# Optimization experiments

Hardware: AMD Instinct MI355X
Metric: run time of the kernel (lower is better)

Reference implementation:

```python
import jax, jax.numpy as jnp
import numpy as np

B, S, E = 2, 2048, 2048
H, D = 16, 128
I = 8192
EPS = 1e-5


def layernorm(x, w, b):
    mu = jnp.mean(x, axis=-1, keepdims=True)
    var = jnp.mean(jnp.square(x - mu), axis=-1, keepdims=True)
    return (x - mu) * jax.lax.rsqrt(var + EPS) * w + b


def setup_inputs() -> dict:
    key = jax.random.key(0)
    ks = jax.random.split(key, 6)
    s = 0.02
    return {
        "x": jax.random.normal(ks[0], (B, S, E), jnp.float32),
        "ln1_w": jnp.ones((E,), jnp.float32),
        "ln1_b": jnp.zeros((E,), jnp.float32),
        "Wqkv": jax.random.normal(ks[1], (E, 3 * E), jnp.float32) * s,
        "Wo": jax.random.normal(ks[2], (E, E), jnp.float32) * s,
        "ln2_w": jnp.ones((E,), jnp.float32),
        "ln2_b": jnp.zeros((E,), jnp.float32),
        "W1": jax.random.normal(ks[3], (E, I), jnp.float32) * s,
        "W2": jax.random.normal(ks[4], (I, E), jnp.float32) * s,
    }


def reference(x, ln1_w, ln1_b, Wqkv, Wo, ln2_w, ln2_b, W1, W2):
    scale = D ** -0.5
    # --- attention sublayer (pre-LN) ---
    h = layernorm(x, ln1_w, ln1_b)
    qkv = (h @ Wqkv).reshape(B, S, 3, H, D)
    q, k, v = [jnp.moveaxis(qkv[:, :, i], 1, 2) for i in range(3)]  # [B,H,S,D]
    scores = jnp.einsum("bhqd,bhkd->bhqk", q, k) * scale
    causal = jnp.triu(jnp.ones((S, S), bool), k=1)
    scores = jnp.where(causal, -jnp.inf, scores)
    attn = jax.nn.softmax(scores, axis=-1)
    out = jnp.einsum("bhqk,bhkd->bqhd", attn, v).reshape(B, S, E)
    x = x + out @ Wo
    # --- FFN sublayer (pre-LN) ---
    h = layernorm(x, ln2_w, ln2_b)
    x = x + jax.nn.gelu(h @ W1, approximate=True) @ W2
    return x
```

## Files before the change

### kernel.cpp

```cpp
#include <hip/hip_runtime.h>
#include <hip/hip_bf16.h>

#define B_ 2
#define S_ 2048
#define E_ 2048
#define H_ 16
#define D_ 128
#define I_ 8192
#define T_ (B_*S_)

typedef __attribute__((ext_vector_type(8))) short bf16x8;
typedef __attribute__((ext_vector_type(8))) unsigned short us8;
typedef __attribute__((ext_vector_type(4))) float f32x4;

__device__ __forceinline__ unsigned short f2bf(float f) {
  union { float f; unsigned int u; } c; c.f = f;
  unsigned int u = c.u;
  unsigned int r = (u + 0x7fffu + ((u >> 16) & 1u)) >> 16;
  return (unsigned short)r;
}

__device__ __forceinline__ void gload16(const void* g, void* l) {
  __builtin_amdgcn_global_load_lds((const __attribute__((address_space(1))) void*)g,
                                   (__attribute__((address_space(3))) void*)l, 16, 0, 0);
}

__global__ void transpose_w(const float* __restrict__ in, unsigned short* __restrict__ out,
                            int K, int N) {
  __shared__ float tile[32][33];
  const int n0 = blockIdx.x * 32, k0 = blockIdx.y * 32;
  const int tx = threadIdx.x, ty = threadIdx.y;
#pragma unroll
  for (int j = 0; j < 4; ++j) {
    int k = k0 + ty + j * 8;
    tile[ty + j * 8][tx] = in[(size_t)k * N + n0 + tx];
  }
  __syncthreads();
#pragma unroll
  for (int j = 0; j < 4; ++j) {
    int n = n0 + ty + j * 8;
    out[(size_t)n * K + k0 + tx] = f2bf(tile[tx][ty + j * 8]);
  }
}

__global__ void ln_kernel(const float* __restrict__ x, const float* __restrict__ w,
                          const float* __restrict__ b, unsigned short* __restrict__ out) {
  const int row = blockIdx.x;
  const int tid = threadIdx.x;
  const int wid = tid >> 6, lane = tid & 63;
  const float4* xr = (const float4*)(x + (size_t)row * E_);
  float4 v0 = xr[tid * 2], v1 = xr[tid * 2 + 1];
  float s  = v0.x + v0.y + v0.z + v0.w + v1.x + v1.y + v1.z + v1.w;
  float sq = v0.x*v0.x + v0.y*v0.y + v0.z*v0.z + v0.w*v0.w
           + v1.x*v1.x + v1.y*v1.y + v1.z*v1.z + v1.w*v1.w;
#pragma unroll
  for (int off = 32; off > 0; off >>= 1) {
    s  += __shfl_xor(s, off);
    sq += __shfl_xor(sq, off);
  }
  __shared__ float red[8];
  if (lane == 0) { red[wid] = s; red[wid + 4] = sq; }
  __syncthreads();
  s  = red[0] + red[1] + red[2] + red[3];
  sq = red[4] + red[5] + red[6] + red[7];
  const float mu  = s * (1.0f / E_);
  const float var = sq * (1.0f / E_) - mu * mu;
  const float rstd = rsqrtf(var + 1e-5f);
  const float4* w4 = (const float4*)w + tid * 2;
  const float4* b4 = (const float4*)b + tid * 2;
  float4 w0 = w4[0], w1 = w4[1], bb0 = b4[0], bb1 = b4[1];
  us8 o;
  o[0] = f2bf((v0.x - mu) * rstd * w0.x + bb0.x);
  o[1] = f2bf((v0.y - mu) * rstd * w0.y + bb0.y);
  o[2] = f2bf((v0.z - mu) * rstd * w0.z + bb0.z);
  o[3] = f2bf((v0.w - mu) * rstd * w0.w + bb0.w);
  o[4] = f2bf((v1.x - mu) * rstd * w1.x + bb1.x);
  o[5] = f2bf((v1.y - mu) * rstd * w1.y + bb1.y);
  o[6] = f2bf((v1.z - mu) * rstd * w1.z + bb1.z);
  o[7] = f2bf((v1.w - mu) * rstd * w1.w + bb1.w);
  *(us8*)(&out[(size_t)row * E_ + tid * 8]) = o;
}

template<int EPI>
__global__ void gemm_bt(const unsigned short* __restrict__ A,
                        const unsigned short* __restrict__ Bt,
                        void* __restrict__ Cout,
                        const float* __restrict__ resid,
                        int M, int N, int K) {
  __shared__ __align__(16) unsigned short As[128 * 32];
  __shared__ __align__(16) unsigned short Bs[128 * 32];
  const int gn = N >> 7;
  const int nwg = (M >> 7) * gn;
  const int cpx = nwg >> 3;
  const int bid = blockIdx.x;
  const int swz = (bid & 7) * cpx + (bid >> 3);
  const int bm = swz / gn, bn = swz % gn;
  const int tid = threadIdx.x;
  const int wid = tid >> 6, lane = tid & 63;
  const int fr = lane & 15, kg = lane >> 4;
  const int wr = wid >> 1, wc = wid & 1;

  const int c0 = wid * 2;
  const unsigned short* gA = A  + (size_t)(bm * 128 + c0 * 16 + (lane >> 2)) * K + (lane & 3) * 8;
  const unsigned short* gB = Bt + (size_t)(bn * 128 + c0 * 16 + (lane >> 2)) * K + (lane & 3) * 8;
  unsigned short* lA = &As[c0 * 512];
  unsigned short* lB = &Bs[c0 * 512];

  const unsigned short* rA = &As[(wr * 64 + fr) * 32 + kg * 8];
  const unsigned short* rB = &Bs[(wc * 64 + fr) * 32 + kg * 8];

  f32x4 acc[4][4] = {};
  const int nk = K >> 5;
  for (int kt = 0; kt < nk; ++kt) {
    __syncthreads();
    gload16(gA,                 lA);
    gload16(gA + 16 * (size_t)K, lA + 512);
    gload16(gB,                 lB);
    gload16(gB + 16 * (size_t)K, lB + 512);
    gA += 32; gB += 32;
    __syncthreads();
    bf16x8 af[4], bfr[4];
#pragma unroll
    for (int m = 0; m < 4; ++m) af[m]  = *(const bf16x8*)(rA + m * 16 * 32);
#pragma unroll
    for (int n = 0; n < 4; ++n) bfr[n] = *(const bf16x8*)(rB + n * 16 * 32);
#pragma unroll
    for (int m = 0; m < 4; ++m)
#pragma unroll
      for (int n = 0; n < 4; ++n)
        acc[m][n] = __builtin_amdgcn_mfma_f32_16x16x32_bf16(af[m], bfr[n], acc[m][n], 0, 0, 0);
  }

  const int row0 = bm * 128 + wr * 64;
  const int col0 = bn * 128 + wc * 64;
#pragma unroll
  for (int m = 0; m < 4; ++m) {
#pragma unroll
    for (int n = 0; n < 4; ++n) {
#pragma unroll
      for (int r = 0; r < 4; ++r) {
        const int row = row0 + m * 16 + kg * 4 + r;
        const int col = col0 + n * 16 + fr;
        const size_t idx = (size_t)row * N + col;
        const float v = acc[m][n][r];
        if constexpr (EPI == 0) {
          ((unsigned short*)Cout)[idx] = f2bf(v);
        } else if constexpr (EPI == 1) {
          const float u = 0.7978845608028654f * (v + 0.044715f * v * v * v);
          const float gel = 0.5f * v * (1.0f + tanhf(u));
          ((unsigned short*)Cout)[idx] = f2bf(gel);
        } else {
          ((float*)Cout)[idx] = v + resid[idx];
        }
      }
    }
  }
}

#define DSR(dst, addr, off) \
  asm volatile("ds_read_b128 %0, %1 offset:%c2" : "=v"(dst) : "v"(addr), "i"(off))
#define LDA4_(aad, kh, mh) \
  DSR(af[0], aad, (kh)*16384 + (mh)*4096 + 0);    \
  DSR(af[1], aad, (kh)*16384 + (mh)*4096 + 1024); \
  DSR(af[2], aad, (kh)*16384 + (mh)*4096 + 2048); \
  DSR(af[3], aad, (kh)*16384 + (mh)*4096 + 3072)
#define LDB4_(bbd, kh) \
  DSR(bq[0], bbd, (kh)*16384 + 0);    \
  DSR(bq[1], bbd, (kh)*16384 + 1024); \
  DSR(bq[2], bbd, (kh)*16384 + 2048); \
  DSR(bq[3], bbd, (kh)*16384 + 3072)
#define FENCE_ do { asm volatile("s_waitcnt lgkmcnt(0)"); \
                    __builtin_amdgcn_sched_barrier(0); } while (0)
#define REG_(op, c, kh) (((((op) * 2 + (c)) * 2 + (kh))) * 8192)

template<int EPI>
__global__ __launch_bounds__(512, 2)
void gemm256(const unsigned short* __restrict__ A,
             const unsigned short* __restrict__ Bt,
             void* __restrict__ Cout,
             const float* __restrict__ resid,
             int M, int N, int K) {
  __shared__ __align__(16) unsigned short lds[65536];
  const int gn = N >> 8;
  const int nwg = (M >> 8) * gn;
  const int cpx = nwg >> 3;
  const int bid = blockIdx.x;
  const int swz = (bid & 7) * cpx + (bid >> 3);
  const int bm = swz / gn, bn = swz % gn;
  const int tid = threadIdx.x;
  const int w = tid >> 6, lane = tid & 63;
  const int fr = lane & 15, kg = lane >> 4;
  const int wr = w >> 2, wc = w & 3;

  const int cc_s = (tid & 7) ^ ((tid >> 3) & 7);
  const int row_s = 2 * (tid >> 3) + (cc_s >> 2);
  const int ks_s = (cc_s & 3) * 8;
  const unsigned short* gA = A  + (size_t)(bm * 256 + row_s) * K + ks_s;
  const unsigned short* gB = Bt + (size_t)(bn * 256 + row_s) * K + ks_s;

  const int lread = (fr >> 1) * 64 + ((((fr & 1) * 4 + kg) ^ (fr >> 1)) * 8);
  const int aA0 = wr * 8192 + lread * 2;
  const int aA1 = 32768 + wr * 8192 + lread * 2;
  const int bB0 = 65536 + wc * 4096 + lread * 2;
  const int bB1 = 65536 + 32768 + wc * 4096 + lread * 2;

  auto STG = [&](const unsigned short* g, unsigned short* l) {
    gload16(g, l);
    gload16(g + (size_t)128 * K, l + 4096);
  };

  f32x4 acc[8][4] = {};
  bf16x8 af[4], bq[4];

  auto MM16 = [&](int mh) {
    __builtin_amdgcn_s_setprio(1);
#pragma unroll
    for (int m = 0; m < 4; ++m)
#pragma unroll
      for (int n = 0; n < 4; ++n)
        acc[mh * 4 + m][n] =
            __builtin_amdgcn_mfma_f32_16x16x32_bf16(af[m], bq[n], acc[mh * 4 + m][n], 0, 0, 0);
    __builtin_amdgcn_s_setprio(0);
  };

#define KTILE(AAD, BBD, DB, kt)  {                                        \
    const bool pf = (kt) + 1 < nk;                                        \
    const unsigned short* gAn = gA + (size_t)((kt) + 1) * 64;             \
    const unsigned short* gBn = gB + (size_t)((kt) + 1) * 64;             \
    LDA4_(AAD, 0, 0); LDB4_(BBD, 0);                                      \
    if (pf) STG(gAn, &lds[REG_(0, DB, 0) + w * 512]);                     \
    __builtin_amdgcn_s_barrier(); FENCE_;                                 \
    MM16(0);                                                              \
    __builtin_amdgcn_s_barrier();                                         \
    LDA4_(AAD, 0, 1);                                                     \
    if (pf) STG(gBn, &lds[REG_(1, DB, 0) + w * 512]);                     \
    __builtin_amdgcn_s_barrier(); FENCE_;                                 \
    MM16(1);                                                              \
    if (pf) { asm volatile("s_waitcnt vmcnt(4)" ::: "memory"); }          \
    else    { asm volatile("s_waitcnt vmcnt(0)" ::: "memory"); }          \
    __builtin_amdgcn_s_barrier();                                         \
    LDA4_(AAD, 1, 0); LDB4_(BBD, 1);                                      \
    if (pf) STG(gAn + 32, &lds[REG_(0, DB, 1) + w * 512]);                \
    __builtin_amdgcn_s_barrier(); FENCE_;                                 \
    MM16(0);                                                              \
    __builtin_amdgcn_s_barrier();                                         \
    LDA4_(AAD, 1, 1);                                                     \
    if (pf) STG(gBn + 32, &lds[REG_(1, DB, 1) + w * 512]);                \
    __builtin_amdgcn_s_barrier(); FENCE_;                                 \
    MM16(1);                                                              \
    if (pf) { asm volatile("s_waitcnt vmcnt(4)" ::: "memory"); }          \
    __builtin_amdgcn_s_barrier();                                         \
  }

  const int nk = K >> 6;
  STG(gA,      &lds[REG_(0, 0, 0) + w * 512]);
  STG(gB,      &lds[REG_(1, 0, 0) + w * 512]);
  STG(gA + 32, &lds[REG_(0, 0, 1) + w * 512]);
  STG(gB + 32, &lds[REG_(1, 0, 1) + w * 512]);
  asm volatile("s_waitcnt vmcnt(4)" ::: "memory");
  __builtin_amdgcn_s_barrier();

  for (int kt2 = 0; kt2 < (nk >> 1); ++kt2) {
    KTILE(aA0, bB0, 1, 2 * kt2);
    KTILE(aA1, bB1, 0, 2 * kt2 + 1);
  }
#undef KTILE

  const int row0 = bm * 256 + wr * 128;
  const int col0 = bn * 256 + wc * 64;
#pragma unroll
  for (int m = 0; m < 8; ++m) {
#pragma unroll
    for (int n = 0; n < 4; ++n) {
#pragma unroll
      for (int r = 0; r < 4; ++r) {
        const int row = row0 + m * 16 + kg * 4 + r;
        const int col = col0 + n * 16 + fr;
        const size_t idx = (size_t)row * N + col;
        const float v = acc[m][n][r];
        if constexpr (EPI == 0) {
          ((unsigned short*)Cout)[idx] = f2bf(v);
        } else if constexpr (EPI == 1) {
          const float u = 0.7978845608028654f * (v + 0.044715f * v * v * v);
          const float gel = 0.5f * v * (1.0f + tanhf(u));
          ((unsigned short*)Cout)[idx] = f2bf(gel);
        } else {
          ((float*)Cout)[idx] = v + resid[idx];
        }
      }
    }
  }
}

__global__ void extract_vT(const unsigned short* __restrict__ qkv, unsigned short* __restrict__ vT) {
  __shared__ unsigned short tile[32][34];
  const int bh = blockIdx.z;
  const int b = bh >> 4, h = bh & 15;
  const int s0 = blockIdx.y * 32, d0 = blockIdx.x * 32;
  const int tx = threadIdx.x, ty = threadIdx.y;
#pragma unroll
  for (int j = 0; j < 4; ++j) {
    int s = s0 + ty + j * 8;
    tile[ty + j * 8][tx] = qkv[(size_t)(b * S_ + s) * 6144 + 4096 + h * 128 + d0 + tx];
  }
  __syncthreads();
#pragma unroll
  for (int j = 0; j < 4; ++j) {
    int d = d0 + ty + j * 8;
    vT[((size_t)bh * 128 + d) * 2048 + s0 + tx] = tile[tx][ty + j * 8];
  }
}

__global__ __launch_bounds__(256, 2)
void attn_kernel(const unsigned short* __restrict__ qkv,
                 const unsigned short* __restrict__ vT,
                 unsigned short* __restrict__ outp) {
  __shared__ __align__(16) unsigned short Ks[64 * 128];
  __shared__ __align__(16) unsigned short Vts[128 * 64];
  __shared__ __align__(16) unsigned short Ps[4 * 16 * 40];
  const int qt = blockIdx.x;
  const int bh = blockIdx.y;
  const int b = bh >> 4, h = bh & 15;
  const int tid = threadIdx.x, wid = tid >> 6, lane = tid & 63;
  const int fr = lane & 15, g = lane >> 4;

  const unsigned short* qptr = qkv + (size_t)(b * S_ + qt * 64 + wid * 16 + fr) * 6144 + h * 128;
  bf16x8 qf[4];
#pragma unroll
  for (int dc = 0; dc < 4; ++dc) qf[dc] = *(const bf16x8*)(qptr + dc * 32 + g * 8);

  float m0[4], l0[4];
#pragma unroll
  for (int r = 0; r < 4; ++r) { m0[r] = -1e30f; l0[r] = 0.0f; }
  f32x4 acc[8] = {};

  const unsigned short* kbase = qkv + (size_t)(b * S_) * 6144 + 2048 + h * 128;
  const unsigned short* vbase = vT + (size_t)bh * 128 * 2048;
  unsigned short* Pw = &Ps[wid * 640];
  const float scale = 0.08838834764831845f;

  us8 kreg[4], vreg[4];
#pragma unroll
  for (int j = 0; j < 4; ++j) {
    const int cc = tid + 256 * j;
    kreg[j] = *(const us8*)(kbase + (size_t)(cc >> 4) * 6144 + (cc & 15) * 8);
    vreg[j] = *(const us8*)(vbase + (size_t)(cc >> 3) * 2048 + (cc & 7) * 8);
  }

  for (int kt = 0; kt <= qt; ++kt) {
    __syncthreads();
#pragma unroll
    for (int j = 0; j < 4; ++j) {
      const int cc = tid + 256 * j;
      const int krow = cc >> 4, kcp = cc & 15;
      *(us8*)(&Ks[krow * 128 + ((kcp * 8) ^ ((krow & 7) << 3))]) = kreg[j];
      const int drow = cc >> 3, vcp = cc & 7;
      *(us8*)(&Vts[drow * 64 + ((vcp * 8) ^ ((drow & 7) << 3))]) = vreg[j];
    }
    if (kt < qt) {
#pragma unroll
      for (int j = 0; j < 4; ++j) {
        const int cc = tid + 256 * j;
        kreg[j] = *(const us8*)(kbase + (size_t)((kt + 1) * 64 + (cc >> 4)) * 6144 + (cc & 15) * 8);
        vreg[j] = *(const us8*)(vbase + (size_t)(cc >> 3) * 2048 + (kt + 1) * 64 + (cc & 7) * 8);
      }
    }
    __syncthreads();

    f32x4 sc[4] = {};
    __builtin_amdgcn_s_setprio(1);
#pragma unroll
    for (int dc = 0; dc < 4; ++dc) {
#pragma unroll
      for (int sub = 0; sub < 4; ++sub) {
        const int row = sub * 16 + fr;
        bf16x8 kf = *(const bf16x8*)(&Ks[row * 128 + ((dc * 32 + g * 8) ^ ((row & 7) << 3))]);
        sc[sub] = __builtin_amdgcn_mfma_f32_16x16x32_bf16(qf[dc], kf, sc[sub], 0, 0, 0);
      }
    }
    __builtin_amdgcn_s_setprio(0);

    float p[4][4];
    const bool diag = (kt == qt);
#pragma unroll
    for (int sub = 0; sub < 4; ++sub) {
#pragma unroll
      for (int r = 0; r < 4; ++r) {
        float v = sc[sub][r] * scale;
        if (diag && (sub * 16 + fr > wid * 16 + g * 4 + r)) v = -1e30f;
        p[sub][r] = v;
      }
    }
    float corr[4];
#pragma unroll
    for (int r = 0; r < 4; ++r) {
      float mx = fmaxf(fmaxf(p[0][r], p[1][r]), fmaxf(p[2][r], p[3][r]));
#pragma unroll
      for (int off = 1; off < 16; off <<= 1) mx = fmaxf(mx, __shfl_xor(mx, off));
      const float mn = fmaxf(m0[r], mx);
      corr[r] = __expf(m0[r] - mn);
      m0[r] = mn;
      float rs = 0.0f;
#pragma unroll
      for (int sub = 0; sub < 4; ++sub) { p[sub][r] = __expf(p[sub][r] - mn); rs += p[sub][r]; }
#pragma unroll
      for (int off = 1; off < 16; off <<= 1) rs += __shfl_xor(rs, off);
      l0[r] = l0[r] * corr[r] + rs;
    }
#pragma unroll
    for (int dt = 0; dt < 8; ++dt)
#pragma unroll
      for (int r = 0; r < 4; ++r) acc[dt][r] *= corr[r];

#pragma unroll
    for (int half = 0; half < 2; ++half) {
#pragma unroll
      for (int s2 = 0; s2 < 2; ++s2)
#pragma unroll
        for (int r = 0; r < 4; ++r)
          Pw[(g * 4 + r) * 40 + s2 * 16 + fr] = f2bf(p[half * 2 + s2][r]);
      bf16x8 pf = *(const bf16x8*)(&Pw[fr * 40 + g * 8]);
      __builtin_amdgcn_s_setprio(1);
#pragma unroll
      for (int dt = 0; dt < 8; ++dt) {
        const int row = dt * 16 + fr;
        bf16x8 vf = *(const bf16x8*)(&Vts[row * 64 + ((half * 32 + g * 8) ^ ((row & 7) << 3))]);
        acc[dt] = __builtin_amdgcn_mfma_f32_16x16x32_bf16(pf, vf, acc[dt], 0, 0, 0);
      }
      __builtin_amdgcn_s_setprio(0);
    }
  }

  float inv[4];
#pragma unroll
  for (int r = 0; r < 4; ++r) inv[r] = 1.0f / l0[r];
#pragma unroll
  for (int dt = 0; dt < 8; ++dt)
#pragma unroll
    for (int r = 0; r < 4; ++r) {
      const size_t row = (size_t)(b * S_ + qt * 64 + wid * 16 + g * 4 + r);
      outp[row * E_ + h * 128 + dt * 16 + fr] = f2bf(acc[dt][r] * inv[r]);
    }
}

extern "C" void kernel_launch(void* const* d_in, const int* in_sizes, int n_in,
                              void* d_out, int out_size, void* d_ws, size_t ws_size,
                              hipStream_t stream) {
  (void)in_sizes; (void)n_in; (void)out_size; (void)ws_size;
  const float* x    = (const float*)d_in[0];
  const float* ln1w = (const float*)d_in[1];
  const float* ln1b = (const float*)d_in[2];
  const float* Wqkv = (const float*)d_in[3];
  const float* Wo   = (const float*)d_in[4];
  const float* ln2w = (const float*)d_in[5];
  const float* ln2b = (const float*)d_in[6];
  const float* W1   = (const float*)d_in[7];
  const float* W2   = (const float*)d_in[8];
  float* out = (float*)d_out;
  char* ws = (char*)d_ws;

  unsigned short* WqkvT = (unsigned short*)(ws + 0);
  unsigned short* WoT   = (unsigned short*)(ws + 25165824);
  unsigned short* W1T   = (unsigned short*)(ws + 33554432);
  unsigned short* W2T   = (unsigned short*)(ws + 67108864);
  unsigned short* qkvb  = (unsigned short*)(ws + 100663296);
  unsigned short* vTb   = (unsigned short*)(ws + 150994944);
  unsigned short* gbuf  = (unsigned short*)(ws + 100663296);
  unsigned short* hbuf  = (unsigned short*)(ws + 167772160);
  float*          x1    = (float*)         (ws + 184549376);

  const dim3 tb(32, 8);
  hipLaunchKernelGGL(transpose_w, dim3(6144 / 32, 2048 / 32), tb, 0, stream, Wqkv, WqkvT, 2048, 6144);
  hipLaunchKernelGGL(transpose_w, dim3(2048 / 32, 2048 / 32), tb, 0, stream, Wo,   WoT,   2048, 2048);
  hipLaunchKernelGGL(transpose_w, dim3(8192 / 32, 2048 / 32), tb, 0, stream, W1,   W1T,   2048, 8192);
  hipLaunchKernelGGL(transpose_w, dim3(2048 / 32, 8192 / 32), tb, 0, stream, W2,   W2T,   8192, 2048);

  hipLaunchKernelGGL(ln_kernel, dim3(T_), dim3(256), 0, stream, x, ln1w, ln1b, hbuf);
  hipLaunchKernelGGL((gemm_bt<0>), dim3(32 * 48), dim3(256), 0, stream,
                     hbuf, WqkvT, (void*)qkvb, (const float*)nullptr, T_, 6144, 2048);
  hipLaunchKernelGGL(extract_vT, dim3(4, 64, 32), tb, 0, stream, qkvb, vTb);
  hipLaunchKernelGGL(attn_kernel, dim3(S_ / 64, B_ * H_), dim3(256), 0, stream, qkvb, vTb, hbuf);
  hipLaunchKernelGGL((gemm_bt<2>), dim3(32 * 16), dim3(256), 0, stream,
                     hbuf, WoT, (void*)x1, x, T_, 2048, 2048);
  hipLaunchKernelGGL(ln_kernel, dim3(T_), dim3(256), 0, stream, x1, ln2w, ln2b, hbuf);
  hipLaunchKernelGGL((gemm256<1>), dim3(16 * 32), dim3(512), 0, stream,
                     hbuf, W1T, (void*)gbuf, (const float*)nullptr, T_, 8192, 2048);
  hipLaunchKernelGGL((gemm_bt<2>), dim3(32 * 16), dim3(256), 0, stream,
                     gbuf, W2T, (void*)out, x1, T_, 2048, 8192);
}
```

Before: 766.3 us.

## Restructure gemm256 into 4-stage k32 ring pipeline; use it for QKV projection

The gemm256 main loop is rebuilt as a four-buffer ring of 32-wide K units with three units prefetched ahead. This removes most of the per-half-tile barriers and uses only a vmcnt wait plus one barrier per unit. The QKV projection is also switched from the 128-tile gemm_bt kernel to the 256x256 gemm256 kernel. The deeper pipeline is meant to hide global-load latency and cut synchronization overhead, but it depends on careful buffer reuse ordering, which could race when a slot is refilled.

```diff
diff --git a/kernel.cpp b/kernel.cpp
--- a/kernel.cpp
+++ b/kernel.cpp
@@ -159,19 +159,6 @@
 
 #define DSR(dst, addr, off) \
   asm volatile("ds_read_b128 %0, %1 offset:%c2" : "=v"(dst) : "v"(addr), "i"(off))
-#define LDA4_(aad, kh, mh) \
-  DSR(af[0], aad, (kh)*16384 + (mh)*4096 + 0);    \
-  DSR(af[1], aad, (kh)*16384 + (mh)*4096 + 1024); \
-  DSR(af[2], aad, (kh)*16384 + (mh)*4096 + 2048); \
-  DSR(af[3], aad, (kh)*16384 + (mh)*4096 + 3072)
-#define LDB4_(bbd, kh) \
-  DSR(bq[0], bbd, (kh)*16384 + 0);    \
-  DSR(bq[1], bbd, (kh)*16384 + 1024); \
-  DSR(bq[2], bbd, (kh)*16384 + 2048); \
-  DSR(bq[3], bbd, (kh)*16384 + 3072)
-#define FENCE_ do { asm volatile("s_waitcnt lgkmcnt(0)"); \
-                    __builtin_amdgcn_sched_barrier(0); } while (0)
-#define REG_(op, c, kh) (((((op) * 2 + (c)) * 2 + (kh))) * 8192)
 
 template<int EPI>
 __global__ __launch_bounds__(512, 2)
@@ -199,15 +186,8 @@
   const unsigned short* gB = Bt + (size_t)(bn * 256 + row_s) * K + ks_s;
 
   const int lread = (fr >> 1) * 64 + ((((fr & 1) * 4 + kg) ^ (fr >> 1)) * 8);
-  const int aA0 = wr * 8192 + lread * 2;
-  const int aA1 = 32768 + wr * 8192 + lread * 2;
-  const int bB0 = 65536 + wc * 4096 + lread * 2;
-  const int bB1 = 65536 + 32768 + wc * 4096 + lread * 2;
-
-  auto STG = [&](const unsigned short* g, unsigned short* l) {
-    gload16(g, l);
-    gload16(g + (size_t)128 * K, l + 4096);
-  };
+  const int la = wr * 8192 + lread * 2;
+  const int lb = 16384 + wc * 4096 + lread * 2;
 
   f32x4 acc[8][4] = {};
   bf16x8 af[4], bq[4];
@@ -222,49 +202,56 @@
             __builtin_amdgcn_mfma_f32_16x16x32_bf16(af[m], bq[n], acc[mh * 4 + m][n], 0, 0, 0);
     __builtin_amdgcn_s_setprio(0);
   };
-
-#define KTILE(AAD, BBD, DB, kt)  {                                        \
-    const bool pf = (kt) + 1 < nk;                                        \
-    const unsigned short* gAn = gA + (size_t)((kt) + 1) * 64;             \
-    const unsigned short* gBn = gB + (size_t)((kt) + 1) * 64;             \
-    LDA4_(AAD, 0, 0); LDB4_(BBD, 0);                                      \
-    if (pf) STG(gAn, &lds[REG_(0, DB, 0) + w * 512]);                     \
-    __builtin_amdgcn_s_barrier(); FENCE_;                                 \
+  auto STGA = [&](int u, int buf) {
+    const unsigned short* g = gA + (size_t)u * 32;
+    unsigned short* d = &lds[buf * 16384 + w * 512];
+    gload16(g, d); gload16(g + (size_t)128 * K, d + 4096);
+  };
+  auto STGB = [&](int u, int buf) {
+    const unsigned short* g = gB + (size_t)u * 32;
+    unsigned short* d = &lds[buf * 16384 + 8192 + w * 512];
+    gload16(g, d); gload16(g + (size_t)128 * K, d + 4096);
+  };
+
+#define UNIT(J, PF, GATE) {                                               \
+    const int aA = la + (J) * 32768;                                      \
+    const int aB = lb + (J) * 32768;                                      \
+    DSR(af[0], aA, 0);    DSR(af[1], aA, 1024);                           \
+    DSR(af[2], aA, 2048); DSR(af[3], aA, 3072);                           \
+    DSR(bq[0], aB, 0);    DSR(bq[1], aB, 1024);                           \
+    DSR(bq[2], aB, 2048); DSR(bq[3], aB, 3072);                           \
+    if (PF) STGA(ku + (J) + 3, ((J) + 3) & 3);                            \
+    asm volatile("s_waitcnt lgkmcnt(0)");                                 \
+    __builtin_amdgcn_sched_barrier(0);                                    \
     MM16(0);                                                              \
-    __builtin_amdgcn_s_barrier();                                         \
-    LDA4_(AAD, 0, 1);                                                     \
-    if (pf) STG(gBn, &lds[REG_(1, DB, 0) + w * 512]);                     \
-    __builtin_amdgcn_s_barrier(); FENCE_;                                 \
+    DSR(af[0], aA, 4096); DSR(af[1], aA, 5120);                           \
+    DSR(af[2], aA, 6144); DSR(af[3], aA, 7168);                           \
+    if (PF) STGB(ku + (J) + 3, ((J) + 3) & 3);                            \
+    asm volatile("s_waitcnt lgkmcnt(0)");                                 \
+    __builtin_amdgcn_sched_barrier(0);                                    \
     MM16(1);                                                              \
-    if (pf) { asm volatile("s_waitcnt vmcnt(4)" ::: "memory"); }          \
-    else    { asm volatile("s_waitcnt vmcnt(0)" ::: "memory"); }          \
-    __builtin_amdgcn_s_barrier();                                         \
-    LDA4_(AAD, 1, 0); LDB4_(BBD, 1);                                      \
-    if (pf) STG(gAn + 32, &lds[REG_(0, DB, 1) + w * 512]);                \
-    __builtin_amdgcn_s_barrier(); FENCE_;                                 \
-    MM16(0);                                                              \
-    __builtin_amdgcn_s_barrier();                                         \
-    LDA4_(AAD, 1, 1);                                                     \
-    if (pf) STG(gBn + 32, &lds[REG_(1, DB, 1) + w * 512]);                \
-    __builtin_amdgcn_s_barrier(); FENCE_;                                 \
-    MM16(1);                                                              \
-    if (pf) { asm volatile("s_waitcnt vmcnt(4)" ::: "memory"); }          \
-    __builtin_amdgcn_s_barrier();                                         \
-  }
-
-  const int nk = K >> 6;
-  STG(gA,      &lds[REG_(0, 0, 0) + w * 512]);
-  STG(gB,      &lds[REG_(1, 0, 0) + w * 512]);
-  STG(gA + 32, &lds[REG_(0, 0, 1) + w * 512]);
-  STG(gB + 32, &lds[REG_(1, 0, 1) + w * 512]);
-  asm volatile("s_waitcnt vmcnt(4)" ::: "memory");
+    if ((GATE) == 8)      asm volatile("s_waitcnt vmcnt(8)" ::: "memory");\
+    else if ((GATE) == 4) asm volatile("s_waitcnt vmcnt(4)" ::: "memory");\
+    else if ((GATE) == 0) asm volatile("s_waitcnt vmcnt(0)" ::: "memory");\
+    if ((GATE) >= 0) __builtin_amdgcn_s_barrier();                        \
+  }
+
+  const int nu = K >> 5;
+  STGA(0, 0); STGB(0, 0);
+  STGA(1, 1); STGB(1, 1);
+  STGA(2, 2); STGB(2, 2);
+  asm volatile("s_waitcnt vmcnt(8)" ::: "memory");
   __builtin_amdgcn_s_barrier();
 
-  for (int kt2 = 0; kt2 < (nk >> 1); ++kt2) {
-    KTILE(aA0, bB0, 1, 2 * kt2);
-    KTILE(aA1, bB1, 0, 2 * kt2 + 1);
-  }
-#undef KTILE
+  int ku = 0;
+  for (int it = 0; it < (nu >> 2) - 1; ++it, ku += 4) {
+    UNIT(0, true, 8); UNIT(1, true, 8); UNIT(2, true, 8); UNIT(3, true, 8);
+  }
+  UNIT(0, true, 8);
+  UNIT(1, false, 4);
+  UNIT(2, false, 0);
+  UNIT(3, false, -1);
+#undef UNIT
 
   const int row0 = bm * 256 + wr * 128;
   const int col0 = bn * 256 + wc * 64;
@@ -476,7 +463,7 @@
   hipLaunchKernelGGL(transpose_w, dim3(2048 / 32, 8192 / 32), tb, 0, stream, W2,   W2T,   8192, 2048);
 
   hipLaunchKernelGGL(ln_kernel, dim3(T_), dim3(256), 0, stream, x, ln1w, ln1b, hbuf);
-  hipLaunchKernelGGL((gemm_bt<0>), dim3(32 * 48), dim3(256), 0, stream,
+  hipLaunchKernelGGL((gemm256<0>), dim3(16 * 24), dim3(512), 0, stream,
                      hbuf, WqkvT, (void*)qkvb, (const float*)nullptr, T_, 6144, 2048);
   hipLaunchKernelGGL(extract_vT, dim3(4, 64, 32), tb, 0, stream, qkvb, vTb);
   hipLaunchKernelGGL(attn_kernel, dim3(S_ / 64, B_ * H_), dim3(256), 0, stream, qkvb, vTb, hbuf);
```

Result: no change. 777.0 us (+1.4%).
